# Optimization experiments

Measured on AMD Instinct MI355X. Metric: run time of the kernel, lower is better.

The kernel has to match this reference:

```python
import jax, jax.numpy as jnp
import numpy as np
from jax import lax

B, H, W = 2, 720, 1280
EPS = 1e-7


def setup_inputs() -> dict:
    key = jax.random.key(0)
    k0, k1, k2, k3, k4, k5 = jax.random.split(key, 6)
    return {
        "img0": jax.random.uniform(k0, (B, 3, H, W), jnp.float32),
        "img1": jax.random.uniform(k1, (B, 3, H, W), jnp.float32),
        "flow0": jax.random.normal(k2, (B, 2, H, W), jnp.float32),
        "flow1": jax.random.normal(k3, (B, 2, H, W), jnp.float32),
        "z0": jax.random.normal(k4, (B, 1, H, W), jnp.float32),
        "z1": jax.random.normal(k5, (B, 1, H, W), jnp.float32),
        "k": 5,
    }


def _softsplat(inp, flow):
    """Forward (splatting) warp. inp [B,C,H,W]; flow [B,2,H,W], ch0 = x-disp, ch1 = y-disp."""
    Bn, C, Hn, Wn = inp.shape
    gx = jnp.arange(Wn, dtype=inp.dtype)
    gy = jnp.arange(Hn, dtype=inp.dtype)
    fx = gx[None, None, :] + flow[:, 0]  # [B,H,W] target x
    fy = gy[None, :, None] + flow[:, 1]  # [B,H,W] target y
    x0 = jnp.floor(fx); x1 = x0 + 1.0
    y0 = jnp.floor(fy); y1 = y0 + 1.0
    # 4 bilinear corners: (x0,y0) (x1,y0) (x0,y1) (x1,y1)
    xs = jnp.stack([x0, x1, x0, x1])            # [4,B,H,W]
    ys = jnp.stack([y0, y0, y1, y1])
    wts = jnp.stack([(x1 - fx) * (y1 - fy),
                     (fx - x0) * (y1 - fy),
                     (x1 - fx) * (fy - y0),
                     (fx - x0) * (fy - y0)])    # [4,B,H,W]
    xi = xs.astype(jnp.int32)
    yi = ys.astype(jnp.int32)
    valid = (xi >= 0) & (xi < Wn) & (yi >= 0) & (yi < Hn)
    wts = jnp.where(valid, wts, 0.0)
    idx = jnp.clip(yi, 0, Hn - 1) * Wn + jnp.clip(xi, 0, Wn - 1)  # [4,B,H,W]
    idx = jnp.moveaxis(idx, 1, 0).reshape(Bn, 4 * Hn * Wn)
    wts = jnp.moveaxis(wts, 1, 0)                                 # [B,4,H,W]

    def splat_one(inp_b, idx_b, w_b):
        # inp_b [C,H,W], idx_b [4HW], w_b [4,H,W]
        vals = (inp_b[None] * w_b[:, None]).transpose(1, 0, 2, 3).reshape(C, 4 * Hn * Wn)
        out = jnp.zeros((C, Hn * Wn), inp_b.dtype)
        out = out.at[:, idx_b].add(vals)
        return out.reshape(C, Hn, Wn)

    return jax.vmap(splat_one)(inp, idx, wts)


def _forewarp_soft(img, flow, metric):
    """flow_forewarp(img, flow, mode='sm', metric=metric, mask=True)."""
    flow = flow[:, ::-1]  # .flip(dims=(1,)) in the original
    Bn, _, Hn, Wn = img.shape
    ones = jnp.ones((Bn, 1, Hn, Wn), img.dtype)
    img_m = jnp.concatenate([img, ones], axis=1)          # mask channel appended
    w = jnp.exp(metric)                                   # softmax-splat weight
    inp = jnp.concatenate([img_m * w, w], axis=1)         # [B, C+2, H, W]
    out = _softsplat(inp, flow)
    return out[:, :-1] / (out[:, -1:] + EPS)              # normalize by splatted weight


def _morph_open(x, k):
    # kornia.morphology.opening with a flat k x k ones SE = min-pool then max-pool
    if k == 0:
        return x
    win = (1, 1, k, k)
    one = (1, 1, 1, 1)
    er = lax.reduce_window(x, jnp.inf, lax.min, win, one, "SAME")
    return lax.reduce_window(er, -jnp.inf, lax.max, win, one, "SAME")


def reference(img0, img1, flow0, flow1, z0, z1, k):
    t = 0.5
    flow0_ = (1.0 - t) * flow0
    flow1_ = t * flow1
    f01 = _forewarp_soft(img0, flow1_, z1)
    f10 = _forewarp_soft(img1, flow0_, z0)
    f01i, f01m = f01[:, :-1], lax.stop_gradient(_morph_open(f01[:, -1:], k))
    f10i, f10m = f10[:, :-1], lax.stop_gradient(_morph_open(f10[:, -1:], k))
    base0 = f01m * f01i + (1.0 - f01m) * f10i
    base1 = f10m * f10i + (1.0 - f10m) * f01i
    # flat concat of ans = [[base0, base1, f01i, f10i], [flow0_, flow1_], [f01m, f10m]] -> 18 ch
    return jnp.concatenate([base0, base1, f01i, f10i, flow0_, flow1_, f01m, f10m], axis=1)
```

## Files before the change

kernel.cpp:

```cpp
#include <hip/hip_runtime.h>
#include <math.h>

#define Hh 720
#define Ww 1280
#define Bb 2
#define HW (Hh*Ww)
#define OUTC 18
#define EPSF 1e-7f

#define DMAX 2.0f
#define OWN_W 32
#define OWN_H 8
#define SRC_W (OWN_W + 5)
#define SRC_H (OWN_H + 5)
#define NSRC (SRC_W * SRC_H)
#define TILES_X (Ww / OWN_W)
#define TILES_Y (Hh / OWN_H)
#define NTILES (Bb * TILES_X * TILES_Y)

#define EW (OWN_W + 4)
#define EH (OWN_H + 4)

__global__ __launch_bounds__(256) void far_prepass_kernel(
    const float* __restrict__ img0, const float* __restrict__ img1,
    const float* __restrict__ flow0, const float* __restrict__ flow1,
    const float* __restrict__ z0, const float* __restrict__ z1,
    float* __restrict__ out, int* __restrict__ flags)
{
    int i = blockIdx.x * 256 + threadIdx.x;
    if (i >= Bb * HW) return;
    int b = i / HW;
    int p = i - b * HW;
    int y = p / Ww;
    int x = p - y * Ww;

    float f1x = flow1[((size_t)b * 2 + 1) * HW + p];
    float f1y = flow1[((size_t)b * 2 + 0) * HW + p];
    float f0x = flow0[((size_t)b * 2 + 1) * HW + p];
    float f0y = flow0[((size_t)b * 2 + 0) * HW + p];
    float dxs[2] = { 0.5f * f1x, 0.5f * f0x };
    float dys[2] = { 0.5f * f1y, 0.5f * f0y };

    out[((size_t)b * OUTC + 14) * HW + p] = 0.5f * f1y;
    out[((size_t)b * OUTC + 15) * HW + p] = 0.5f * f1x;

    for (int d = 0; d < 2; ++d) {
        float dx = dxs[d], dy = dys[d];
        if (fabsf(dx) <= DMAX && fabsf(dy) <= DMAX) continue;

        const float* img = d ? img1 : img0;
        const float* met = d ? z0 : z1;
        float fx = (float)x + dx;
        float fy = (float)y + dy;
        float w  = expf(met[(size_t)b * HW + p]);
        float v0 = img[((size_t)b * 3 + 0) * HW + p] * w;
        float v1 = img[((size_t)b * 3 + 1) * HW + p] * w;
        float v2 = img[((size_t)b * 3 + 2) * HW + p] * w;

        float x0f = floorf(fx), y0f = floorf(fy);
        float x1f = x0f + 1.0f, y1f = y0f + 1.0f;
        int   x0  = (int)x0f,  y0i = (int)y0f;
        float wxs[2] = { x1f - fx, fx - x0f };
        float wys[2] = { y1f - fy, fy - y0f };

        float* accImg = out + ((size_t)b * OUTC + (d ? 9 : 6)) * HW;
        float* accW   = out + ((size_t)b * OUTC + (d ? 17 : 16)) * HW;

        for (int cy = 0; cy < 2; ++cy) {
            int yy = y0i + cy;
            if (yy < 0 || yy >= Hh) continue;
            for (int cx = 0; cx < 2; ++cx) {
                int xx = x0 + cx;
                if (xx < 0 || xx >= Ww) continue;
                float wt = wxs[cx] * wys[cy];
                if (wt == 0.0f) continue;
                int q = yy * Ww + xx;
                atomicAdd(accImg + q,          v0 * wt);
                atomicAdd(accImg + HW + q,     v1 * wt);
                atomicAdd(accImg + 2 * HW + q, v2 * wt);
                atomicAdd(accW + q,            w  * wt);
                if (flags)
                    flags[(b * TILES_Y + yy / OWN_H) * TILES_X + xx / OWN_W] = 1;
            }
        }
    }
}

__global__ __launch_bounds__(256) void gather_splat_kernel(
    const float* __restrict__ img0, const float* __restrict__ img1,
    const float* __restrict__ flow0, const float* __restrict__ flow1,
    const float* __restrict__ z0, const float* __restrict__ z1,
    float* __restrict__ out, const int* __restrict__ flags)
{
    __shared__ float4 geo[SRC_H][SRC_W];
    __shared__ float4 vw [SRC_H][SRC_W];

    int wg   = blockIdx.x;
    int wgid = (wg & 7) * (NTILES / 8) + (wg >> 3);
    int b    = wgid / (TILES_X * TILES_Y);
    int rr   = wgid - b * (TILES_X * TILES_Y);
    int tY   = rr / TILES_X;
    int tX   = rr - tY * TILES_X;
    const int tX0 = tX * OWN_W;
    const int tY0 = tY * OWN_H;

    const int qlx = threadIdx.x & (OWN_W - 1);
    const int qly = threadIdx.x >> 5;

    float acc[2][4];
#pragma unroll
    for (int d = 0; d < 2; ++d)
#pragma unroll
        for (int c = 0; c < 4; ++c) acc[d][c] = 0.0f;

#pragma unroll
    for (int d = 0; d < 2; ++d) {
        if (d) __syncthreads();

        const float* flw = d ? flow0 : flow1;
        const float* met = d ? z0 : z1;
        const float* img = d ? img1 : img0;

        for (int c = threadIdx.x; c < NSRC; c += 256) {
            int cy = c / SRC_W, cx = c - cy * SRC_W;
            int sx = tX0 + cx - 2;
            int sy = tY0 + cy - 2;
            bool inimg = (sx >= 0) && (sx < Ww) && (sy >= 0) && (sy < Hh);
            int p = min(max(sy, 0), Hh - 1) * Ww + min(max(sx, 0), Ww - 1);

            float fxv = flw[((size_t)b * 2 + 1) * HW + p];
            float fyv = flw[((size_t)b * 2 + 0) * HW + p];
            float zz  = met[(size_t)b * HW + p];
            float i0  = img[((size_t)b * 3 + 0) * HW + p];
            float i1  = img[((size_t)b * 3 + 1) * HW + p];
            float i2  = img[((size_t)b * 3 + 2) * HW + p];

            float dx = 0.5f * fxv, dy = 0.5f * fyv;
            bool l = inimg && (fabsf(dx) <= DMAX) && (fabsf(dy) <= DMAX);
            float w = l ? expf(zz) : 0.0f;

            float fx = (float)sx + dx, fy = (float)sy + dy;
            float x0f = floorf(fx), y0f = floorf(fy);
            geo[cy][cx] = make_float4(l ? x0f - (float)sx : 1e9f,
                                      l ? y0f - (float)sy : 1e9f,
                                      fx - x0f, fy - y0f);
            vw[cy][cx] = make_float4(i0 * w, i1 * w, i2 * w, w);
        }
        __syncthreads();

#pragma unroll
        for (int oy = 0; oy < 6; ++oy) {
            const float oyf = (float)(oy - 2);
#pragma unroll
            for (int ox = 0; ox < 6; ++ox) {
                const float oxf = (float)(ox - 2);
                float4 g = geo[qly + oy][qlx + ox];
                float tx = g.x + oxf;
                float ty = g.y + oyf;
                float wx = (tx == 0.0f) ? (1.0f - g.z) : ((tx == -1.0f) ? g.z : 0.0f);
                float wy = (ty == 0.0f) ? (1.0f - g.w) : ((ty == -1.0f) ? g.w : 0.0f);
                float wt = wx * wy;
                if (wt > 0.0f) {
                    float4 v = vw[qly + oy][qlx + ox];
                    acc[d][0] += wt * v.x;
                    acc[d][1] += wt * v.y;
                    acc[d][2] += wt * v.z;
                    acc[d][3] += wt * v.w;
                }
            }
        }
    }

    const size_t q = (size_t)(tY0 + qly) * Ww + (tX0 + qlx);
    bool flagged = true;
    if (flags)
        flagged = flags[(b * TILES_Y + tY) * TILES_X + tX] != 0;

#pragma unroll
    for (int d = 0; d < 2; ++d) {
        float* accImg = out + ((size_t)b * OUTC + (d ? 9 : 6)) * HW;
        float* accW   = out + ((size_t)b * OUTC + (d ? 17 : 16)) * HW;
        float s0 = acc[d][0];
        float s1 = acc[d][1];
        float s2 = acc[d][2];
        float sw = acc[d][3];
        if (flagged) {
            s0 += accImg[q];
            s1 += accImg[HW + q];
            s2 += accImg[2 * HW + q];
            sw += accW[q];
        }
        float inv = 1.0f / (sw + EPSF);
        accImg[q]          = s0 * inv;
        accImg[HW + q]     = s1 * inv;
        accImg[2 * HW + q] = s2 * inv;
        accW[q]            = sw;
    }
}

__global__ __launch_bounds__(256) void erode5_kernel(float* __restrict__ out,
                                                     const int* __restrict__ kptr)
{
    __shared__ float s2  [2][EH][EW];
    __shared__ float rmin[2][EH][OWN_W];

    int k = *kptr;
    if (k > 5) return;

    int wg   = blockIdx.x;
    int wgid = (wg & 7) * (NTILES / 8) + (wg >> 3);
    int b    = wgid / (TILES_X * TILES_Y);
    int rr   = wgid - b * (TILES_X * TILES_Y);
    int tY   = rr / TILES_X;
    int tX   = rr - tY * TILES_X;
    const int tX0 = tX * OWN_W;
    const int tY0 = tY * OWN_H;

    const float* s01 = out + ((size_t)b * OUTC + 16) * HW;
    const float* s10 = out + ((size_t)b * OUTC + 17) * HW;
    float* er01 = out + ((size_t)b * OUTC + 12) * HW;
    float* er10 = out + ((size_t)b * OUTC + 13) * HW;

    const int r  = threadIdx.x >> 5;
    const int xc = threadIdx.x & 31;
    const size_t qp = (size_t)(tY0 + r) * Ww + (tX0 + xc);

    if (k <= 0) { er01[qp] = s01[qp]; er10[qp] = s10[qp]; return; }

    const int lo = (k - 1) / 2;
    const int ew = OWN_W + k - 1;
    const int eh = OWN_H + k - 1;

    for (int c = threadIdx.x; c < eh * ew; c += 256) {
        int i = c / ew, j = c - i * ew;
        int gy = min(max(tY0 - lo + i, 0), Hh - 1);
        int gx = min(max(tX0 - lo + j, 0), Ww - 1);
        size_t p = (size_t)gy * Ww + gx;
        s2[0][i][j] = s01[p];
        s2[1][i][j] = s10[p];
    }
    __syncthreads();

    for (int c = threadIdx.x; c < eh * OWN_W; c += 256) {
        int i = c / OWN_W, x = c - i * OWN_W;
        float m0 = s2[0][i][x], m1 = s2[1][i][x];
        for (int t = 1; t < k; ++t) {
            m0 = fminf(m0, s2[0][i][x + t]);
            m1 = fminf(m1, s2[1][i][x + t]);
        }
        rmin[0][i][x] = m0;
        rmin[1][i][x] = m1;
    }
    __syncthreads();

    float m0 = rmin[0][r][xc], m1 = rmin[1][r][xc];
    for (int t = 1; t < k; ++t) {
        m0 = fminf(m0, rmin[0][r + t][xc]);
        m1 = fminf(m1, rmin[1][r + t][xc]);
    }
    er01[qp] = m0;
    er10[qp] = m1;
}

__global__ __launch_bounds__(256) void fuse5_kernel(float* __restrict__ out,
                                                    const int* __restrict__ kptr)
{
    __shared__ float e2  [2][EH][EW];
    __shared__ float rmax[2][EH][OWN_W];

    int k = *kptr;
    if (k > 5) return;

    int wg   = blockIdx.x;
    int wgid = (wg & 7) * (NTILES / 8) + (wg >> 3);
    int b    = wgid / (TILES_X * TILES_Y);
    int rr   = wgid - b * (TILES_X * TILES_Y);
    int tY   = rr / TILES_X;
    int tX   = rr - tY * TILES_X;
    const int tX0 = tX * OWN_W;
    const int tY0 = tY * OWN_H;

    const float* er01 = out + ((size_t)b * OUTC + 12) * HW;
    const float* er10 = out + ((size_t)b * OUTC + 13) * HW;

    const int r  = threadIdx.x >> 5;
    const int xc = threadIdx.x & 31;
    const size_t qp = (size_t)(tY0 + r) * Ww + (tX0 + xc);

    float o0, o1;
    if (k <= 0) {
        o0 = er01[qp];
        o1 = er10[qp];
    } else {
        const int lo = (k - 1) / 2;
        const int ew = OWN_W + k - 1;
        const int eh = OWN_H + k - 1;

        for (int c = threadIdx.x; c < eh * ew; c += 256) {
            int i = c / ew, j = c - i * ew;
            int gy = min(max(tY0 - lo + i, 0), Hh - 1);
            int gx = min(max(tX0 - lo + j, 0), Ww - 1);
            size_t p = (size_t)gy * Ww + gx;
            e2[0][i][j] = er01[p];
            e2[1][i][j] = er10[p];
        }
        __syncthreads();

        for (int c = threadIdx.x; c < eh * OWN_W; c += 256) {
            int i = c / OWN_W, x = c - i * OWN_W;
            float m0 = e2[0][i][x], m1 = e2[1][i][x];
            for (int t = 1; t < k; ++t) {
                m0 = fmaxf(m0, e2[0][i][x + t]);
                m1 = fmaxf(m1, e2[1][i][x + t]);
            }
            rmax[0][i][x] = m0;
            rmax[1][i][x] = m1;
        }
        __syncthreads();

        o0 = rmax[0][r][xc]; o1 = rmax[1][r][xc];
        for (int t = 1; t < k; ++t) {
            o0 = fmaxf(o0, rmax[0][r + t][xc]);
            o1 = fmaxf(o1, rmax[1][r + t][xc]);
        }
    }

    float m01 = o0 / (o0 + EPSF);
    float m10 = o1 / (o1 + EPSF);

    float* ob = out + (size_t)b * OUTC * HW;
#pragma unroll
    for (int c = 0; c < 3; ++c) {
        float f01i = ob[((size_t)6 + c) * HW + qp];
        float f10i = ob[((size_t)9 + c) * HW + qp];
        ob[((size_t)0 + c) * HW + qp] = m01 * f01i + (1.0f - m01) * f10i;
        ob[((size_t)3 + c) * HW + qp] = m10 * f10i + (1.0f - m10) * f01i;
    }
    ob[(size_t)16 * HW + qp] = m01;
    ob[(size_t)17 * HW + qp] = m10;
}

__global__ __launch_bounds__(256) void erode_kernel(float* __restrict__ out,
                                                    const int* __restrict__ kptr)
{
    int k = *kptr;
    if (k <= 5) return;
    int i = blockIdx.x * 256 + threadIdx.x;
    if (i >= Bb * HW) return;
    int b = i / HW;
    int p = i - b * HW;
    int y = p / Ww;
    int x = p - y * Ww;

    const float* s01 = out + ((size_t)b * OUTC + 16) * HW;
    const float* s10 = out + ((size_t)b * OUTC + 17) * HW;
    float* er01 = out + ((size_t)b * OUTC + 12) * HW;
    float* er10 = out + ((size_t)b * OUTC + 13) * HW;

    int lo = (k - 1) / 2, hi = (k - 1) - lo;
    float m0 = INFINITY, m1 = INFINITY;
    for (int dy = -lo; dy <= hi; ++dy) {
        int yy = y + dy;
        if (yy < 0 || yy >= Hh) continue;
        for (int dx = -lo; dx <= hi; ++dx) {
            int xx = x + dx;
            if (xx < 0 || xx >= Ww) continue;
            int q = yy * Ww + xx;
            m0 = fminf(m0, s01[q]);
            m1 = fminf(m1, s10[q]);
        }
    }
    er01[p] = m0;
    er10[p] = m1;
}

__global__ __launch_bounds__(256) void fuse_kernel(float* __restrict__ out,
                                                   const int* __restrict__ kptr)
{
    int k = *kptr;
    if (k <= 5) return;
    int i = blockIdx.x * 256 + threadIdx.x;
    if (i >= Bb * HW) return;
    int b = i / HW;
    int p = i - b * HW;
    int y = p / Ww;
    int x = p - y * Ww;

    const float* er01 = out + ((size_t)b * OUTC + 12) * HW;
    const float* er10 = out + ((size_t)b * OUTC + 13) * HW;

    int lo = (k - 1) / 2, hi = (k - 1) - lo;
    float o0 = -INFINITY, o1 = -INFINITY;
    for (int dy = -lo; dy <= hi; ++dy) {
        int yy = y + dy;
        if (yy < 0 || yy >= Hh) continue;
        for (int dx = -lo; dx <= hi; ++dx) {
            int xx = x + dx;
            if (xx < 0 || xx >= Ww) continue;
            int q = yy * Ww + xx;
            o0 = fmaxf(o0, er01[q]);
            o1 = fmaxf(o1, er10[q]);
        }
    }

    float m01 = o0 / (o0 + EPSF);
    float m10 = o1 / (o1 + EPSF);

    float* ob = out + (size_t)b * OUTC * HW;
#pragma unroll
    for (int c = 0; c < 3; ++c) {
        float f01i = ob[((size_t)6 + c) * HW + p];
        float f10i = ob[((size_t)9 + c) * HW + p];
        ob[((size_t)0 + c) * HW + p] = m01 * f01i + (1.0f - m01) * f10i;
        ob[((size_t)3 + c) * HW + p] = m10 * f10i + (1.0f - m10) * f01i;
    }
    ob[(size_t)16 * HW + p] = m01;
    ob[(size_t)17 * HW + p] = m10;
}

__global__ __launch_bounds__(256) void flow_kernel(const float* __restrict__ flow0,
                                                   float* __restrict__ out)
{
    int i = blockIdx.x * 256 + threadIdx.x;
    if (i >= Bb * 2 * HW) return;
    int b = i / (2 * HW);
    int r = i - b * 2 * HW;
    int c = r / HW;
    int p = r - c * HW;
    out[((size_t)b * OUTC + 12 + c) * HW + p] = 0.5f * flow0[((size_t)b * 2 + c) * HW + p];
}

extern "C" void kernel_launch(void* const* d_in, const int* in_sizes, int n_in,
                              void* d_out, int out_size, void* d_ws, size_t ws_size,
                              hipStream_t stream) {
    const float* img0  = (const float*)d_in[0];
    const float* img1  = (const float*)d_in[1];
    const float* flow0 = (const float*)d_in[2];
    const float* flow1 = (const float*)d_in[3];
    const float* z0    = (const float*)d_in[4];
    const float* z1    = (const float*)d_in[5];
    const int*   kptr  = (const int*)d_in[6];
    float* out = (float*)d_out;

    for (int b = 0; b < Bb; ++b) {
        hipMemsetAsync(out + ((size_t)b * OUTC + 6) * HW, 0, (size_t)6 * HW * sizeof(float), stream);
        hipMemsetAsync(out + ((size_t)b * OUTC + 16) * HW, 0, (size_t)2 * HW * sizeof(float), stream);
    }

    int* flags = nullptr;
    if (d_ws && ws_size >= (size_t)NTILES * sizeof(int)) {
        flags = (int*)d_ws;
        hipMemsetAsync(flags, 0, (size_t)NTILES * sizeof(int), stream);
    }

    int n = Bb * HW;
    int blocks = (n + 255) / 256;

    far_prepass_kernel<<<blocks, 256, 0, stream>>>(img0, img1, flow0, flow1, z0, z1, out, flags);
    gather_splat_kernel<<<NTILES, 256, 0, stream>>>(img0, img1, flow0, flow1, z0, z1, out, flags);
    erode5_kernel<<<NTILES, 256, 0, stream>>>(out, kptr);
    erode_kernel<<<blocks, 256, 0, stream>>>(out, kptr);
    fuse5_kernel<<<NTILES, 256, 0, stream>>>(out, kptr);
    fuse_kernel<<<blocks, 256, 0, stream>>>(out, kptr);
    int n2 = Bb * 2 * HW;
    flow_kernel<<<(n2 + 255) / 256, 256, 0, stream>>>(flow0, out);
}
```

Baseline: 302.5 us.

## Consolidate launches, merge gather source loads, move erosion to workspace

Five memset calls are replaced by a single vectorized zero kernel. The separate generic erode and fuse kernels are folded into the tiled k<=5 kernels, and when workspace is available the flow0 output copy moves into the prepass so flow_kernel is skipped. The eroded masks then go to a workspace buffer instead of output channels 12-13. The gather kernel now stages both directions' source tiles into shared memory in one pass with a single barrier, which doubles LDS use per block and may reduce occupancy. The aim is to cut launch and memset overhead and the extra synchronisation in gather.

```diff
diff --git a/kernel.cpp b/kernel.cpp
--- a/kernel.cpp
+++ b/kernel.cpp
@@ -21,11 +21,31 @@
 #define EW (OWN_W + 4)
 #define EH (OWN_H + 4)
 
+__global__ __launch_bounds__(256) void zero_kernel(float* __restrict__ out,
+                                                   int* __restrict__ flags)
+{
+    size_t idx = (size_t)blockIdx.x * 256 + threadIdx.x;
+    if (flags) {
+        for (size_t f = idx; f < NTILES; f += (size_t)gridDim.x * 256)
+            flags[f] = 0;
+    }
+    const size_t n4 = (size_t)Bb * 8 * HW / 4;
+    for (size_t i = idx; i < n4; i += (size_t)gridDim.x * 256) {
+        size_t e = i * 4;
+        int b = (int)(e / ((size_t)8 * HW));
+        size_t r = e - (size_t)b * 8 * HW;
+        int c = (int)(r / HW);
+        size_t p = r - (size_t)c * HW;
+        int ch = (c < 6) ? (6 + c) : (16 + (c - 6));
+        *(float4*)(out + ((size_t)b * OUTC + ch) * HW + p) = make_float4(0.f, 0.f, 0.f, 0.f);
+    }
+}
+
 __global__ __launch_bounds__(256) void far_prepass_kernel(
     const float* __restrict__ img0, const float* __restrict__ img1,
     const float* __restrict__ flow0, const float* __restrict__ flow1,
     const float* __restrict__ z0, const float* __restrict__ z1,
-    float* __restrict__ out, int* __restrict__ flags)
+    float* __restrict__ out, int* __restrict__ flags, int wf01)
 {
     int i = blockIdx.x * 256 + threadIdx.x;
     if (i >= Bb * HW) return;
@@ -43,6 +63,10 @@
 
     out[((size_t)b * OUTC + 14) * HW + p] = 0.5f * f1y;
     out[((size_t)b * OUTC + 15) * HW + p] = 0.5f * f1x;
+    if (wf01) {
+        out[((size_t)b * OUTC + 12) * HW + p] = 0.5f * f0y;
+        out[((size_t)b * OUTC + 13) * HW + p] = 0.5f * f0x;
+    }
 
     for (int d = 0; d < 2; ++d) {
         float dx = dxs[d], dy = dys[d];
@@ -92,8 +116,8 @@
     const float* __restrict__ z0, const float* __restrict__ z1,
     float* __restrict__ out, const int* __restrict__ flags)
 {
-    __shared__ float4 geo[SRC_H][SRC_W];
-    __shared__ float4 vw [SRC_H][SRC_W];
+    __shared__ float4 geo[2][SRC_H][SRC_W];
+    __shared__ float4 vw [2][SRC_H][SRC_W];
 
     int wg   = blockIdx.x;
     int wgid = (wg & 7) * (NTILES / 8) + (wg >> 3);
@@ -104,6 +128,49 @@
     const int tX0 = tX * OWN_W;
     const int tY0 = tY * OWN_H;
 
+    for (int c = threadIdx.x; c < NSRC; c += 256) {
+        int cy = c / SRC_W, cx = c - cy * SRC_W;
+        int sx = tX0 + cx - 2;
+        int sy = tY0 + cy - 2;
+        bool inimg = (sx >= 0) && (sx < Ww) && (sy >= 0) && (sy < Hh);
+        int p = min(max(sy, 0), Hh - 1) * Ww + min(max(sx, 0), Ww - 1);
+
+        float f1x = flow1[((size_t)b * 2 + 1) * HW + p];
+        float f1y = flow1[((size_t)b * 2 + 0) * HW + p];
+        float f0x = flow0[((size_t)b * 2 + 1) * HW + p];
+        float f0y = flow0[((size_t)b * 2 + 0) * HW + p];
+        float zz1 = z1[(size_t)b * HW + p];
+        float zz0 = z0[(size_t)b * HW + p];
+        float a0 = img0[((size_t)b * 3 + 0) * HW + p];
+        float a1 = img0[((size_t)b * 3 + 1) * HW + p];
+        float a2 = img0[((size_t)b * 3 + 2) * HW + p];
+        float c0 = img1[((size_t)b * 3 + 0) * HW + p];
+        float c1 = img1[((size_t)b * 3 + 1) * HW + p];
+        float c2 = img1[((size_t)b * 3 + 2) * HW + p];
+
+        float dx0 = 0.5f * f1x, dy0 = 0.5f * f1y;
+        float dx1 = 0.5f * f0x, dy1 = 0.5f * f0y;
+        bool l0 = inimg && (fabsf(dx0) <= DMAX) && (fabsf(dy0) <= DMAX);
+        bool l1 = inimg && (fabsf(dx1) <= DMAX) && (fabsf(dy1) <= DMAX);
+        float w0 = l0 ? expf(zz1) : 0.0f;
+        float w1 = l1 ? expf(zz0) : 0.0f;
+
+        float fx0 = (float)sx + dx0, fy0 = (float)sy + dy0;
+        float fx1 = (float)sx + dx1, fy1 = (float)sy + dy1;
+        float x0f0 = floorf(fx0), y0f0 = floorf(fy0);
+        float x0f1 = floorf(fx1), y0f1 = floorf(fy1);
+
+        geo[0][cy][cx] = make_float4(l0 ? x0f0 - (float)sx : 1e9f,
+                                     l0 ? y0f0 - (float)sy : 1e9f,
+                                     fx0 - x0f0, fy0 - y0f0);
+        geo[1][cy][cx] = make_float4(l1 ? x0f1 - (float)sx : 1e9f,
+                                     l1 ? y0f1 - (float)sy : 1e9f,
+                                     fx1 - x0f1, fy1 - y0f1);
+        vw[0][cy][cx] = make_float4(a0 * w0, a1 * w0, a2 * w0, w0);
+        vw[1][cy][cx] = make_float4(c0 * w1, c1 * w1, c2 * w1, w1);
+    }
+    __syncthreads();
+
     const int qlx = threadIdx.x & (OWN_W - 1);
     const int qly = threadIdx.x >> 5;
 
@@ -115,53 +182,20 @@
 
 #pragma unroll
     for (int d = 0; d < 2; ++d) {
-        if (d) __syncthreads();
-
-        const float* flw = d ? flow0 : flow1;
-        const float* met = d ? z0 : z1;
-        const float* img = d ? img1 : img0;
-
-        for (int c = threadIdx.x; c < NSRC; c += 256) {
-            int cy = c / SRC_W, cx = c - cy * SRC_W;
-            int sx = tX0 + cx - 2;
-            int sy = tY0 + cy - 2;
-            bool inimg = (sx >= 0) && (sx < Ww) && (sy >= 0) && (sy < Hh);
-            int p = min(max(sy, 0), Hh - 1) * Ww + min(max(sx, 0), Ww - 1);
-
-            float fxv = flw[((size_t)b * 2 + 1) * HW + p];
-            float fyv = flw[((size_t)b * 2 + 0) * HW + p];
-            float zz  = met[(size_t)b * HW + p];
-            float i0  = img[((size_t)b * 3 + 0) * HW + p];
-            float i1  = img[((size_t)b * 3 + 1) * HW + p];
-            float i2  = img[((size_t)b * 3 + 2) * HW + p];
-
-            float dx = 0.5f * fxv, dy = 0.5f * fyv;
-            bool l = inimg && (fabsf(dx) <= DMAX) && (fabsf(dy) <= DMAX);
-            float w = l ? expf(zz) : 0.0f;
-
-            float fx = (float)sx + dx, fy = (float)sy + dy;
-            float x0f = floorf(fx), y0f = floorf(fy);
-            geo[cy][cx] = make_float4(l ? x0f - (float)sx : 1e9f,
-                                      l ? y0f - (float)sy : 1e9f,
-                                      fx - x0f, fy - y0f);
-            vw[cy][cx] = make_float4(i0 * w, i1 * w, i2 * w, w);
-        }
-        __syncthreads();
-
 #pragma unroll
         for (int oy = 0; oy < 6; ++oy) {
             const float oyf = (float)(oy - 2);
 #pragma unroll
             for (int ox = 0; ox < 6; ++ox) {
                 const float oxf = (float)(ox - 2);
-                float4 g = geo[qly + oy][qlx + ox];
+                float4 g = geo[d][qly + oy][qlx + ox];
                 float tx = g.x + oxf;
                 float ty = g.y + oyf;
                 float wx = (tx == 0.0f) ? (1.0f - g.z) : ((tx == -1.0f) ? g.z : 0.0f);
                 float wy = (ty == 0.0f) ? (1.0f - g.w) : ((ty == -1.0f) ? g.w : 0.0f);
                 float wt = wx * wy;
                 if (wt > 0.0f) {
-                    float4 v = vw[qly + oy][qlx + ox];
+                    float4 v = vw[d][qly + oy][qlx + ox];
                     acc[d][0] += wt * v.x;
                     acc[d][1] += wt * v.y;
                     acc[d][2] += wt * v.z;
@@ -198,14 +232,42 @@
     }
 }
 
-__global__ __launch_bounds__(256) void erode5_kernel(float* __restrict__ out,
+__global__ __launch_bounds__(256) void erode5_kernel(float* out, float* erbuf,
+                                                     int er_in_out,
                                                      const int* __restrict__ kptr)
 {
     __shared__ float s2  [2][EH][EW];
     __shared__ float rmin[2][EH][OWN_W];
 
     int k = *kptr;
-    if (k > 5) return;
+
+    if (k > 5) {
+        int i = blockIdx.x * 256 + threadIdx.x;
+        int b = i / HW;
+        int p = i - b * HW;
+        int y = p / Ww;
+        int x = p - y * Ww;
+        const float* s01 = out + ((size_t)b * OUTC + 16) * HW;
+        const float* s10 = out + ((size_t)b * OUTC + 17) * HW;
+        float* er01 = er_in_out ? out + ((size_t)b * OUTC + 12) * HW : erbuf + ((size_t)b * 2 + 0) * HW;
+        float* er10 = er_in_out ? out + ((size_t)b * OUTC + 13) * HW : erbuf + ((size_t)b * 2 + 1) * HW;
+        int lo = (k - 1) / 2, hi = (k - 1) - lo;
+        float m0 = INFINITY, m1 = INFINITY;
+        for (int dy = -lo; dy <= hi; ++dy) {
+            int yy = y + dy;
+            if (yy < 0 || yy >= Hh) continue;
+            for (int dx = -lo; dx <= hi; ++dx) {
+                int xx = x + dx;
+                if (xx < 0 || xx >= Ww) continue;
+                int q = yy * Ww + xx;
+                m0 = fminf(m0, s01[q]);
+                m1 = fminf(m1, s10[q]);
+            }
+        }
+        er01[p] = m0;
+        er10[p] = m1;
+        return;
+    }
 
     int wg   = blockIdx.x;
     int wgid = (wg & 7) * (NTILES / 8) + (wg >> 3);
@@ -218,8 +280,8 @@
 
     const float* s01 = out + ((size_t)b * OUTC + 16) * HW;
     const float* s10 = out + ((size_t)b * OUTC + 17) * HW;
-    float* er01 = out + ((size_t)b * OUTC + 12) * HW;
-    float* er10 = out + ((size_t)b * OUTC + 13) * HW;
+    float* er01 = er_in_out ? out + ((size_t)b * OUTC + 12) * HW : erbuf + ((size_t)b * 2 + 0) * HW;
+    float* er10 = er_in_out ? out + ((size_t)b * OUTC + 13) * HW : erbuf + ((size_t)b * 2 + 1) * HW;
 
     const int r  = threadIdx.x >> 5;
     const int xc = threadIdx.x & 31;
@@ -262,14 +324,50 @@
     er10[qp] = m1;
 }
 
-__global__ __launch_bounds__(256) void fuse5_kernel(float* __restrict__ out,
+__global__ __launch_bounds__(256) void fuse5_kernel(float* out, const float* erbuf,
+                                                    int er_in_out,
                                                     const int* __restrict__ kptr)
 {
     __shared__ float e2  [2][EH][EW];
     __shared__ float rmax[2][EH][OWN_W];
 
     int k = *kptr;
-    if (k > 5) return;
+
+    if (k > 5) {
+        int i = blockIdx.x * 256 + threadIdx.x;
+        int b = i / HW;
+        int p = i - b * HW;
+        int y = p / Ww;
+        int x = p - y * Ww;
+        const float* er01 = er_in_out ? out + ((size_t)b * OUTC + 12) * HW : erbuf + ((size_t)b * 2 + 0) * HW;
+        const float* er10 = er_in_out ? out + ((size_t)b * OUTC + 13) * HW : erbuf + ((size_t)b * 2 + 1) * HW;
+        int lo = (k - 1) / 2, hi = (k - 1) - lo;
+        float o0 = -INFINITY, o1 = -INFINITY;
+        for (int dy = -lo; dy <= hi; ++dy) {
+            int yy = y + dy;
+            if (yy < 0 || yy >= Hh) continue;
+            for (int dx = -lo; dx <= hi; ++dx) {
+                int xx = x + dx;
+                if (xx < 0 || xx >= Ww) continue;
+                int q = yy * Ww + xx;
+                o0 = fmaxf(o0, er01[q]);
+                o1 = fmaxf(o1, er10[q]);
+            }
+        }
+        float m01 = o0 / (o0 + EPSF);
+        float m10 = o1 / (o1 + EPSF);
+        float* ob = out + (size_t)b * OUTC * HW;
+#pragma unroll
+        for (int c = 0; c < 3; ++c) {
+            float f01i = ob[((size_t)6 + c) * HW + p];
+            float f10i = ob[((size_t)9 + c) * HW + p];
+            ob[((size_t)0 + c) * HW + p] = m01 * f01i + (1.0f - m01) * f10i;
+            ob[((size_t)3 + c) * HW + p] = m10 * f10i + (1.0f - m10) * f01i;
+        }
+        ob[(size_t)16 * HW + p] = m01;
+        ob[(size_t)17 * HW + p] = m10;
+        return;
+    }
 
     int wg   = blockIdx.x;
     int wgid = (wg & 7) * (NTILES / 8) + (wg >> 3);
@@ -280,8 +378,8 @@
     const int tX0 = tX * OWN_W;
     const int tY0 = tY * OWN_H;
 
-    const float* er01 = out + ((size_t)b * OUTC + 12) * HW;
-    const float* er10 = out + ((size_t)b * OUTC + 13) * HW;
+    const float* er01 = er_in_out ? out + ((size_t)b * OUTC + 12) * HW : erbuf + ((size_t)b * 2 + 0) * HW;
+    const float* er10 = er_in_out ? out + ((size_t)b * OUTC + 13) * HW : erbuf + ((size_t)b * 2 + 1) * HW;
 
     const int r  = threadIdx.x >> 5;
     const int xc = threadIdx.x & 31;
@@ -338,84 +436,6 @@
     }
     ob[(size_t)16 * HW + qp] = m01;
     ob[(size_t)17 * HW + qp] = m10;
-}
-
-__global__ __launch_bounds__(256) void erode_kernel(float* __restrict__ out,
-                                                    const int* __restrict__ kptr)
-{
-    int k = *kptr;
-    if (k <= 5) return;
-    int i = blockIdx.x * 256 + threadIdx.x;
-    if (i >= Bb * HW) return;
-    int b = i / HW;
-    int p = i - b * HW;
-    int y = p / Ww;
-    int x = p - y * Ww;
-
-    const float* s01 = out + ((size_t)b * OUTC + 16) * HW;
-    const float* s10 = out + ((size_t)b * OUTC + 17) * HW;
-    float* er01 = out + ((size_t)b * OUTC + 12) * HW;
-    float* er10 = out + ((size_t)b * OUTC + 13) * HW;
-
-    int lo = (k - 1) / 2, hi = (k - 1) - lo;
-    float m0 = INFINITY, m1 = INFINITY;
-    for (int dy = -lo; dy <= hi; ++dy) {
-        int yy = y + dy;
-        if (yy < 0 || yy >= Hh) continue;
-        for (int dx = -lo; dx <= hi; ++dx) {
-            int xx = x + dx;
-            if (xx < 0 || xx >= Ww) continue;
-            int q = yy * Ww + xx;
-            m0 = fminf(m0, s01[q]);
-            m1 = fminf(m1, s10[q]);
-        }
-    }
-    er01[p] = m0;
-    er10[p] = m1;
-}
-
-__global__ __launch_bounds__(256) void fuse_kernel(float* __restrict__ out,
-                                                   const int* __restrict__ kptr)
-{
-    int k = *kptr;
-    if (k <= 5) return;
-    int i = blockIdx.x * 256 + threadIdx.x;
-    if (i >= Bb * HW) return;
-    int b = i / HW;
-    int p = i - b * HW;
-    int y = p / Ww;
-    int x = p - y * Ww;
-
-    const float* er01 = out + ((size_t)b * OUTC + 12) * HW;
-    const float* er10 = out + ((size_t)b * OUTC + 13) * HW;
-
-    int lo = (k - 1) / 2, hi = (k - 1) - lo;
-    float o0 = -INFINITY, o1 = -INFINITY;
-    for (int dy = -lo; dy <= hi; ++dy) {
-        int yy = y + dy;
-        if (yy < 0 || yy >= Hh) continue;
-        for (int dx = -lo; dx <= hi; ++dx) {
-            int xx = x + dx;
-            if (xx < 0 || xx >= Ww) continue;
-            int q = yy * Ww + xx;
-            o0 = fmaxf(o0, er01[q]);
-            o1 = fmaxf(o1, er10[q]);
-        }
-    }
-
-    float m01 = o0 / (o0 + EPSF);
-    float m10 = o1 / (o1 + EPSF);
-
-    float* ob = out + (size_t)b * OUTC * HW;
-#pragma unroll
-    for (int c = 0; c < 3; ++c) {
-        float f01i = ob[((size_t)6 + c) * HW + p];
-        float f10i = ob[((size_t)9 + c) * HW + p];
-        ob[((size_t)0 + c) * HW + p] = m01 * f01i + (1.0f - m01) * f10i;
-        ob[((size_t)3 + c) * HW + p] = m10 * f10i + (1.0f - m10) * f01i;
-    }
-    ob[(size_t)16 * HW + p] = m01;
-    ob[(size_t)17 * HW + p] = m10;
 }
 
 __global__ __launch_bounds__(256) void flow_kernel(const float* __restrict__ flow0,
@@ -442,26 +462,22 @@
     const int*   kptr  = (const int*)d_in[6];
     float* out = (float*)d_out;
 
-    for (int b = 0; b < Bb; ++b) {
-        hipMemsetAsync(out + ((size_t)b * OUTC + 6) * HW, 0, (size_t)6 * HW * sizeof(float), stream);
-        hipMemsetAsync(out + ((size_t)b * OUTC + 16) * HW, 0, (size_t)2 * HW * sizeof(float), stream);
-    }
-
-    int* flags = nullptr;
-    if (d_ws && ws_size >= (size_t)NTILES * sizeof(int)) {
-        flags = (int*)d_ws;
-        hipMemsetAsync(flags, 0, (size_t)NTILES * sizeof(int), stream);
-    }
-
-    int n = Bb * HW;
-    int blocks = (n + 255) / 256;
-
-    far_prepass_kernel<<<blocks, 256, 0, stream>>>(img0, img1, flow0, flow1, z0, z1, out, flags);
+    const size_t flagsBytes = (((size_t)NTILES * sizeof(int)) + 255) & ~(size_t)255;
+    const size_t erBytes    = (size_t)Bb * 2 * HW * sizeof(float);
+
+    int*   flags = (d_ws && ws_size >= (size_t)NTILES * sizeof(int)) ? (int*)d_ws : nullptr;
+    bool   wsmode = d_ws && ws_size >= flagsBytes + erBytes;
+    float* erbuf  = wsmode ? (float*)((char*)d_ws + flagsBytes) : nullptr;
+    int    er_in_out = wsmode ? 0 : 1;
+
+    zero_kernel<<<2048, 256, 0, stream>>>(out, flags);
+    far_prepass_kernel<<<NTILES, 256, 0, stream>>>(img0, img1, flow0, flow1, z0, z1,
+                                                   out, flags, wsmode ? 1 : 0);
     gather_splat_kernel<<<NTILES, 256, 0, stream>>>(img0, img1, flow0, flow1, z0, z1, out, flags);
-    erode5_kernel<<<NTILES, 256, 0, stream>>>(out, kptr);
-    erode_kernel<<<blocks, 256, 0, stream>>>(out, kptr);
-    fuse5_kernel<<<NTILES, 256, 0, stream>>>(out, kptr);
-    fuse_kernel<<<blocks, 256, 0, stream>>>(out, kptr);
-    int n2 = Bb * 2 * HW;
-    flow_kernel<<<(n2 + 255) / 256, 256, 0, stream>>>(flow0, out);
-}
+    erode5_kernel<<<NTILES, 256, 0, stream>>>(out, erbuf, er_in_out, kptr);
+    fuse5_kernel<<<NTILES, 256, 0, stream>>>(out, erbuf, er_in_out, kptr);
+    if (!wsmode) {
+        int n2 = Bb * 2 * HW;
+        flow_kernel<<<(n2 + 255) / 256, 256, 0, stream>>>(flow0, out);
+    }
+}
```

After: 294.6 us. 2.6% less time.
